# Kernel tuning notes

Measured on AMD Instinct MI355X. Metric: run time of the kernel, lower is better.

Reference implementation:

```python
import jax, jax.numpy as jnp
import numpy as np

EMBED = 1024
HEADS = 16
HEAD_DIM = EMBED // HEADS


def setup_inputs() -> dict:
    key = jax.random.key(0)
    ks = jax.random.split(key, 5)
    s = 0.02
    x = jax.random.normal(ks[0], (2, 2048, EMBED), dtype=jnp.float32)
    W_qkv = jax.random.normal(ks[1], (EMBED, 3 * EMBED), dtype=jnp.float32) * s
    b_qkv = jnp.zeros((3 * EMBED,), dtype=jnp.float32)
    W_proj = jax.random.normal(ks[2], (EMBED, EMBED), dtype=jnp.float32) * s
    b_proj = jnp.zeros((EMBED,), dtype=jnp.float32)
    return {"x": x, "W_qkv": W_qkv, "b_qkv": b_qkv, "W_proj": W_proj, "b_proj": b_proj}


def reference(x, W_qkv, b_qkv, W_proj, b_proj):
    B, N, _ = x.shape
    scale = HEAD_DIM ** -0.5
    qkv = x @ W_qkv + b_qkv                     # [B,N,3E]
    qkv = qkv.reshape(B, N, 3, HEADS, HEAD_DIM)
    q = qkv[:, :, 0].transpose(0, 2, 1, 3) * scale  # [B,H,N,D]
    k = qkv[:, :, 1].transpose(0, 2, 1, 3)
    v = qkv[:, :, 2].transpose(0, 2, 1, 3)
    attn = jnp.einsum('bhnd,bhmd->bhnm', q, k)  # [B,H,N,N]
    attn = jax.nn.softmax(attn, axis=-1)
    out = jnp.einsum('bhnm,bhmd->bhnd', attn, v)  # [B,H,N,D]
    out = out.transpose(0, 2, 1, 3).reshape(B, N, HEADS * HEAD_DIM)
    return out @ W_proj + b_proj
```

## Files before the change

### kernel.cpp

```cpp
#include <hip/hip_runtime.h>
#include <hip/hip_bf16.h>
#include <stdint.h>

typedef unsigned short u16;
typedef __bf16 bf16x8 __attribute__((ext_vector_type(8)));
typedef float f32x4 __attribute__((ext_vector_type(4)));
typedef float f32x16 __attribute__((ext_vector_type(16)));

__device__ __forceinline__ u16 f2bf(float f) {
    union { float f; unsigned u; } x; x.f = f;
    unsigned u = x.u;
    u += 0x7FFFu + ((u >> 16) & 1u);
    return (u16)(u >> 16);
}
__device__ __forceinline__ float bf2f(u16 h) {
    union { unsigned u; float f; } x; x.u = ((unsigned)h) << 16; return x.f;
}

typedef __attribute__((address_space(1))) void gvoid;
typedef __attribute__((address_space(3))) void lvoid;
__device__ __forceinline__ void gl2lds16(const void* g, void* l) {
    __builtin_amdgcn_global_load_lds((gvoid*)g, (lvoid*)l, 16, 0, 0);
}

__global__ __launch_bounds__(256) void prep_kernel(
    const float* __restrict__ x, u16* __restrict__ xb,
    const float* __restrict__ Wqkv, u16* __restrict__ wqkvT,
    const float* __restrict__ Wproj, u16* __restrict__ wprojT)
{
    __shared__ u16 tile[64][65];
    const int blk = blockIdx.x;
    const int tid = threadIdx.x;

    if (blk < 2048) {
        const size_t i = ((size_t)blk * 256 + tid) * 8;
        float4 a = *(const float4*)(x + i);
        float4 b = *(const float4*)(x + i + 4);
        ushort4 oa, ob;
        oa.x = f2bf(a.x); oa.y = f2bf(a.y); oa.z = f2bf(a.z); oa.w = f2bf(a.w);
        ob.x = f2bf(b.x); ob.y = f2bf(b.y); ob.z = f2bf(b.z); ob.w = f2bf(b.w);
        *(ushort4*)(xb + i) = oa;
        *(ushort4*)(xb + i + 4) = ob;
        return;
    }
    const float* in; u16* out; int rows, cols, bx, by;
    if (blk < 2816) { int t = blk - 2048; in = Wqkv;  out = wqkvT;  rows = 1024; cols = 3072; bx = t % 48; by = t / 48; }
    else            { int t = blk - 2816; in = Wproj; out = wprojT; rows = 1024; cols = 1024; bx = t % 16; by = t / 16; }
#pragma unroll
    for (int i = 0; i < 16; i++) {
        int e = i * 256 + tid;
        int r = e >> 6, c = e & 63;
        tile[r][c] = f2bf(in[(size_t)(by * 64 + r) * cols + bx * 64 + c]);
    }
    __syncthreads();
#pragma unroll
    for (int i = 0; i < 16; i++) {
        int e = i * 256 + tid;
        int r = e >> 6, c = e & 63;
        out[(size_t)(bx * 64 + r) * rows + by * 64 + c] = tile[c][r];
    }
}

__global__ __launch_bounds__(256) void gemm_qkv(
    const u16* __restrict__ A, const u16* __restrict__ Bt,
    const float* __restrict__ bias,
    u16* __restrict__ q, u16* __restrict__ ko, u16* __restrict__ vt)
{
    constexpr int K = 1024;
    __shared__ __align__(16) u16 smem[64 * 64 + 128 * 64];
    u16* sA = smem;
    u16* sB = smem + 4096;
    const int tid = threadIdx.x;
    const int wave = tid >> 6, lane = tid & 63;
    const int quad = lane >> 4, l16 = lane & 15;
    const int wm = (wave >> 1) * 32, wn = (wave & 1) * 64;
    const int m0 = blockIdx.y * 64, n0 = blockIdx.x * 128;
    const int srow = lane >> 3;
    const int scolz = ((lane & 7) ^ srow) * 8;

    f32x4 acc[2][4];
#pragma unroll
    for (int i = 0; i < 2; i++)
#pragma unroll
        for (int j = 0; j < 4; j++)
#pragma unroll
            for (int r = 0; r < 4; r++) acc[i][j][r] = 0.f;

    for (int kt = 0; kt < K; kt += 64) {
        __syncthreads();
#pragma unroll
        for (int t = 0; t < 2; t++) {
            int rb = wave * 16 + t * 8;
            gl2lds16(A + (size_t)(m0 + rb + srow) * K + kt + scolz, &sA[rb * 64]);
        }
#pragma unroll
        for (int t = 0; t < 4; t++) {
            int rb = wave * 32 + t * 8;
            gl2lds16(Bt + (size_t)(n0 + rb + srow) * K + kt + scolz, &sB[rb * 64]);
        }
        __syncthreads();
#pragma unroll
        for (int kk = 0; kk < 64; kk += 32) {
            bf16x8 af[2], bfr[4];
            int sl = (((kk >> 3) + quad) ^ (l16 & 7)) * 8;
#pragma unroll
            for (int t = 0; t < 2; t++)
                af[t] = *(const bf16x8*)&sA[(wm + t * 16 + l16) * 64 + sl];
#pragma unroll
            for (int t = 0; t < 4; t++)
                bfr[t] = *(const bf16x8*)&sB[(wn + t * 16 + l16) * 64 + sl];
#pragma unroll
            for (int i = 0; i < 2; i++)
#pragma unroll
                for (int j = 0; j < 4; j++)
                    acc[i][j] = __builtin_amdgcn_mfma_f32_16x16x32_bf16(
                        af[i], bfr[j], acc[i][j], 0, 0, 0);
        }
    }

    const float QSCALE = 0.18033688011112042f;
    const float sc = (n0 < 1024) ? QSCALE : 1.0f;
    __syncthreads();
#pragma unroll
    for (int i = 0; i < 2; i++) {
#pragma unroll
        for (int j = 0; j < 4; j++) {
            float bv = bias[n0 + wn + j * 16 + l16];
#pragma unroll
            for (int r = 0; r < 4; r++) {
                float v = (acc[i][j][r] + bv) * sc;
                smem[(wm + i * 16 + quad * 4 + r) * 132 + wn + j * 16 + l16] = f2bf(v);
            }
        }
    }
    __syncthreads();

    if (n0 < 2048) {
        u16* dst = (n0 < 1024) ? q : ko;
#pragma unroll
        for (int it = 0; it < 4; it++) {
            int c = it * 256 + tid;
            int m_l = c >> 4;
            int n8 = (c & 15) * 8;
            uint4 w = *(const uint4*)&smem[m_l * 132 + n8];
            int n = n0 + n8;
            int h = (n & 1023) >> 6, d = n & 63;
            int m = m0 + m_l;
            int b = m >> 11, t = m & 2047;
            *(uint4*)(dst + ((size_t)(b * 16 + h) * 2048 + t) * 64 + d) = w;
        }
    } else {
        constexpr int PERM[16] = {0,1,2,3, 8,9,10,11, 4,5,6,7, 12,13,14,15};
        int nv = n0 - 2048;
        int n_l = tid & 127, mh = tid >> 7;
        int hh = (nv >> 6) + (n_l >> 6);
        int d = n_l & 63;
        int bb = m0 >> 11, t0 = m0 & 2047;
        u16* vrow = vt + ((size_t)(bb * 16 + hh) * 64 + d) * 2048 + t0 + mh * 32;
#pragma unroll
        for (int it = 0; it < 4; it++) {
            int base = mh * 32 + it * 8;
            union { u16 s[8]; uint4 w; } pk;
#pragma unroll
            for (int i = 0; i < 8; i++) {
                int pos = base + i;
                int row = (pos & ~15) | PERM[pos & 15];
                pk.s[i] = smem[row * 132 + n_l];
            }
            *(uint4*)(vrow + it * 8) = pk.w;
        }
    }
}

__global__ __launch_bounds__(256, 4) void attn_kernel(
    const u16* __restrict__ q, const u16* __restrict__ ko,
    const u16* __restrict__ vt,
    u16* __restrict__ op0, u16* __restrict__ op1,
    float* __restrict__ lp0, float* __restrict__ lp1)
{
    __shared__ __align__(16) u16 sK[2][64 * 72];
    __shared__ __align__(16) u16 sV[2][64 * 72];

    const int tid = threadIdx.x;
    const int wave = tid >> 6, lane = tid & 63;
    const int l31 = lane & 31, hi = lane >> 5;

    const int lid = blockIdx.x;
    const int xcd = lid & 7, idx = lid >> 3;
    const int h = xcd * 2 + (idx & 1);
    const int b = (idx >> 1) & 1;
    const int q0 = ((idx >> 2) & 15) * 128;
    const int khalf = idx >> 6;
    const int kbase = khalf * 1024;
    const size_t bh = (size_t)(b * 16 + h);

    const u16* qp  = q  + bh * 2048 * 64;
    const u16* kp  = ko + bh * 2048 * 64;
    const u16* vtp = vt + bh * 64 * 2048;

    bf16x8 qf[4];
    {
        const u16* qrow = qp + (size_t)(q0 + wave * 32 + l31) * 64 + hi * 8;
#pragma unroll
        for (int d = 0; d < 4; d++)
            qf[d] = *(const bf16x8*)(qrow + d * 16);
    }

    const int sr0 = tid >> 3;
    const int sc0 = (tid & 7) * 8;
    const int sr1 = sr0 + 32;

    uint4 pk0 = *(const uint4*)(kp + (size_t)(kbase + sr0) * 64 + sc0);
    uint4 pk1 = *(const uint4*)(kp + (size_t)(kbase + sr1) * 64 + sc0);
    uint4 pv0 = *(const uint4*)(vtp + (size_t)sr0 * 2048 + kbase + sc0);
    uint4 pv1 = *(const uint4*)(vtp + (size_t)sr1 * 2048 + kbase + sc0);

    f32x16 accO[2];
#pragma unroll
    for (int d = 0; d < 2; d++)
#pragma unroll
        for (int r = 0; r < 16; r++) accO[d][r] = 0.f;
    float ls[4] = {0.f, 0.f, 0.f, 0.f};

    for (int t = 0; t < 16; ++t) {
        const int cur = t & 1;
        u16* sKc = &sK[cur][0];
        u16* sVc = &sV[cur][0];
        *(uint4*)&sKc[sr0 * 72 + sc0] = pk0;
        *(uint4*)&sKc[sr1 * 72 + sc0] = pk1;
        *(uint4*)&sVc[sr0 * 72 + sc0] = pv0;
        *(uint4*)&sVc[sr1 * 72 + sc0] = pv1;
        if (t < 15) {
            int nt = kbase + (t + 1) * 64;
            pk0 = *(const uint4*)(kp + (size_t)(nt + sr0) * 64 + sc0);
            pk1 = *(const uint4*)(kp + (size_t)(nt + sr1) * 64 + sc0);
            pv0 = *(const uint4*)(vtp + (size_t)sr0 * 2048 + nt + sc0);
            pv1 = *(const uint4*)(vtp + (size_t)sr1 * 2048 + nt + sc0);
        }
        __syncthreads();

#pragma unroll
        for (int rb = 0; rb < 2; rb++) {
            f32x16 S;
#pragma unroll
            for (int r = 0; r < 16; r++) S[r] = 0.f;
            const u16* krd = &sKc[(rb * 32 + l31) * 72 + hi * 8];
#pragma unroll
            for (int d = 0; d < 4; d++) {
                bf16x8 kf = *(const bf16x8*)(krd + d * 16);
                S = __builtin_amdgcn_mfma_f32_32x32x16_bf16(kf, qf[d], S, 0, 0, 0);
            }
            union { float f; unsigned u; } e[16];
#pragma unroll
            for (int r = 0; r < 16; r++) {
                e[r].f = __builtin_amdgcn_exp2f(S[r]);
                ls[r & 3] += e[r].f;
            }
#pragma unroll
            for (int ks2 = 0; ks2 < 2; ks2++) {
                union { unsigned u[4]; bf16x8 v; } pa;
#pragma unroll
                for (int s = 0; s < 4; s++) {
                    unsigned r0 = e[ks2 * 8 + 2 * s].u + 0x8000u;
                    unsigned r1 = e[ks2 * 8 + 2 * s + 1].u + 0x8000u;
                    pa.u[s] = (r1 & 0xFFFF0000u) | (r0 >> 16);
                }
                const int nb = rb * 32 + ks2 * 16 + hi * 8;
#pragma unroll
                for (int db = 0; db < 2; db++) {
                    bf16x8 vf = *(const bf16x8*)&sVc[(db * 32 + l31) * 72 + nb];
                    accO[db] = __builtin_amdgcn_mfma_f32_32x32x16_bf16(pa.v, vf, accO[db], 0, 0, 0);
                }
            }
        }
    }

    u16* op = khalf ? op1 : op0;
    float* lp = khalf ? lp1 : lp0;

    float lsum = (ls[0] + ls[1]) + (ls[2] + ls[3]);
    float ltot = lsum + __shfl_xor(lsum, 32, 64);
    int qq0 = q0 + wave * 32;
    if (hi == 0) lp[bh * 2048 + qq0 + l31] = ltot;

#pragma unroll
    for (int db = 0; db < 2; db++)
#pragma unroll
        for (int r = 0; r < 16; r++) {
            int tq = qq0 + (r & 3) + 8 * (r >> 2) + 4 * hi;
            size_t row = (size_t)b * 2048 + tq;
            op[row * 1024 + h * 64 + db * 32 + l31] = f2bf(accO[db][r]);
        }
}

__global__ __launch_bounds__(256) void combine_kernel(
    const u16* __restrict__ op0, const u16* __restrict__ op1,
    const float* __restrict__ lp0, const float* __restrict__ lp1,
    u16* __restrict__ ob)
{
    const size_t i = ((size_t)blockIdx.x * 256 + threadIdx.x) * 8;
    int m = (int)(i >> 10), e = (int)(i & 1023);
    int b = m >> 11, t = m & 2047, h = e >> 6;
    float inv = 1.f / (lp0[(size_t)(b * 16 + h) * 2048 + t] +
                       lp1[(size_t)(b * 16 + h) * 2048 + t]);
    union { uint4 w; u16 s[8]; } a, c, o;
    a.w = *(const uint4*)(op0 + i);
    c.w = *(const uint4*)(op1 + i);
#pragma unroll
    for (int k = 0; k < 8; k++)
        o.s[k] = f2bf((bf2f(a.s[k]) + bf2f(c.s[k])) * inv);
    *(uint4*)(ob + i) = o.w;
}

__global__ __launch_bounds__(256) void gemm_proj(
    const u16* __restrict__ A, const u16* __restrict__ Bt,
    const float* __restrict__ bias, float* __restrict__ out)
{
    constexpr int K = 1024;
    __shared__ __align__(16) u16 sA[32 * 64];
    __shared__ __align__(16) u16 sB[128 * 64];
    const int tid = threadIdx.x;
    const int wave = tid >> 6, lane = tid & 63;
    const int quad = lane >> 4, l16 = lane & 15;
    const int wn = wave * 32;

    const int lid = blockIdx.x;
    const int xcd = lid & 7, idx = lid >> 3;
    const int m0 = (xcd * 16 + (idx & 15)) * 32;
    const int n0 = (idx >> 4) * 128;

    const int srow = lane >> 3;
    const int scolz = ((lane & 7) ^ srow) * 8;

    f32x4 acc[2][2];
#pragma unroll
    for (int i = 0; i < 2; i++)
#pragma unroll
        for (int j = 0; j < 2; j++)
#pragma unroll
            for (int r = 0; r < 4; r++) acc[i][j][r] = 0.f;

    for (int kt = 0; kt < K; kt += 64) {
        __syncthreads();
        {
            int rb = wave * 8;
            gl2lds16(A + (size_t)(m0 + rb + srow) * K + kt + scolz, &sA[rb * 64]);
        }
#pragma unroll
        for (int t = 0; t < 4; t++) {
            int rb = wave * 32 + t * 8;
            gl2lds16(Bt + (size_t)(n0 + rb + srow) * K + kt + scolz, &sB[rb * 64]);
        }
        __syncthreads();
#pragma unroll
        for (int kk = 0; kk < 64; kk += 32) {
            bf16x8 af[2], bfr[2];
            int sl = (((kk >> 3) + quad) ^ (l16 & 7)) * 8;
#pragma unroll
            for (int t = 0; t < 2; t++)
                af[t] = *(const bf16x8*)&sA[(t * 16 + l16) * 64 + sl];
#pragma unroll
            for (int t = 0; t < 2; t++)
                bfr[t] = *(const bf16x8*)&sB[(wn + t * 16 + l16) * 64 + sl];
#pragma unroll
            for (int i = 0; i < 2; i++)
#pragma unroll
                for (int j = 0; j < 2; j++)
                    acc[i][j] = __builtin_amdgcn_mfma_f32_16x16x32_bf16(
                        af[i], bfr[j], acc[i][j], 0, 0, 0);
        }
    }

#pragma unroll
    for (int i = 0; i < 2; i++) {
#pragma unroll
        for (int j = 0; j < 2; j++) {
            int n = n0 + wn + j * 16 + l16;
            float bv = bias[n];
#pragma unroll
            for (int r = 0; r < 4; r++) {
                int m = m0 + i * 16 + quad * 4 + r;
                out[(size_t)m * 1024 + n] = acc[i][j][r] + bv;
            }
        }
    }
}

extern "C" void kernel_launch(void* const* d_in, const int* in_sizes, int n_in,
                              void* d_out, int out_size, void* d_ws, size_t ws_size,
                              hipStream_t stream) {
    const float* x     = (const float*)d_in[0];
    const float* Wqkv  = (const float*)d_in[1];
    const float* bqkv  = (const float*)d_in[2];
    const float* Wproj = (const float*)d_in[3];
    const float* bproj = (const float*)d_in[4];
    float* out = (float*)d_out;
    char* ws = (char*)d_ws;

    u16* wqkvT  = (u16*)(ws);
    u16* wprojT = (u16*)(ws +  6291456);
    u16* xb     = (u16*)(ws +  8388608);
    u16* qb     = (u16*)(ws + 16777216);
    u16* kb     = (u16*)(ws + 25165824);
    u16* vtb    = (u16*)(ws + 33554432);
    u16* ob     = (u16*)(ws + 41943040);

    u16*   op0 = ob;
    u16*   op1 = xb;
    float* lp0 = (float*)wqkvT;
    float* lp1 = (float*)(ws + 262144);

    prep_kernel<<<dim3(3072), 256, 0, stream>>>(x, xb, Wqkv, wqkvT, Wproj, wprojT);
    gemm_qkv<<<dim3(24, 64), 256, 0, stream>>>(xb, wqkvT, bqkv, qb, kb, vtb);
    attn_kernel<<<dim3(1024), 256, 0, stream>>>(qb, kb, vtb, op0, op1, lp0, lp1);
    combine_kernel<<<dim3(2048), 256, 0, stream>>>(op0, op1, lp0, lp1, ob);
    gemm_proj<<<dim3(1024), 256, 0, stream>>>(ob, wprojT, bproj, out);
}
```

Before: 185.7 us.

## Fuse split-K combine into attention kernel via per-tile arrival counter

Drops the separate combine kernel. Each attention block bumps an atomic counter for its query tile after writing its partial output and row sum. The second block to arrive reads the other half's partial output and row sums, then writes the normalized bf16 result straight into the projection input. This removes one kernel launch and one full pass over both partial buffers. In exchange it adds a counter memset, thread fences, and scattered 2-byte global loads and stores in the attention epilogue.

After: 285.4 us. 1.54x slower.

```diff
diff --git a/kernel.cpp b/kernel.cpp
--- a/kernel.cpp
+++ b/kernel.cpp
@@ -176,10 +176,12 @@
     const u16* __restrict__ q, const u16* __restrict__ ko,
     const u16* __restrict__ vt,
     u16* __restrict__ op0, u16* __restrict__ op1,
-    float* __restrict__ lp0, float* __restrict__ lp1)
+    float* __restrict__ lp0, float* __restrict__ lp1,
+    int* __restrict__ cnt, u16* __restrict__ obf)
 {
     __shared__ __align__(16) u16 sK[2][64 * 72];
     __shared__ __align__(16) u16 sV[2][64 * 72];
+    __shared__ int sOld;
 
     const int tid = threadIdx.x;
     const int wave = tid >> 6, lane = tid & 63;
@@ -189,10 +191,12 @@
     const int xcd = lid & 7, idx = lid >> 3;
     const int h = xcd * 2 + (idx & 1);
     const int b = (idx >> 1) & 1;
-    const int q0 = ((idx >> 2) & 15) * 128;
+    const int qt = (idx >> 2) & 15;
+    const int q0 = qt * 128;
     const int khalf = idx >> 6;
     const int kbase = khalf * 1024;
     const size_t bh = (size_t)(b * 16 + h);
+    const int tileid = (int)bh * 16 + qt;
 
     const u16* qp  = q  + bh * 2048 * 64;
     const u16* kp  = ko + bh * 2048 * 64;
@@ -291,25 +295,32 @@
             size_t row = (size_t)b * 2048 + tq;
             op[row * 1024 + h * 64 + db * 32 + l31] = f2bf(accO[db][r]);
         }
-}
-
-__global__ __launch_bounds__(256) void combine_kernel(
-    const u16* __restrict__ op0, const u16* __restrict__ op1,
-    const float* __restrict__ lp0, const float* __restrict__ lp1,
-    u16* __restrict__ ob)
-{
-    const size_t i = ((size_t)blockIdx.x * 256 + threadIdx.x) * 8;
-    int m = (int)(i >> 10), e = (int)(i & 1023);
-    int b = m >> 11, t = m & 2047, h = e >> 6;
-    float inv = 1.f / (lp0[(size_t)(b * 16 + h) * 2048 + t] +
-                       lp1[(size_t)(b * 16 + h) * 2048 + t]);
-    union { uint4 w; u16 s[8]; } a, c, o;
-    a.w = *(const uint4*)(op0 + i);
-    c.w = *(const uint4*)(op1 + i);
-#pragma unroll
-    for (int k = 0; k < 8; k++)
-        o.s[k] = f2bf((bf2f(a.s[k]) + bf2f(c.s[k])) * inv);
-    *(uint4*)(ob + i) = o.w;
+
+    __syncthreads();
+    if (tid == 0) {
+        __threadfence();
+        sOld = atomicAdd(&cnt[tileid], 1);
+    }
+    __syncthreads();
+    if (sOld == 0) return;
+
+    __threadfence();
+    const u16*   oo = khalf ? op0 : op1;
+    const float* lo = khalf ? lp0 : lp1;
+    float lot = lo[bh * 2048 + qq0 + l31];
+
+#pragma unroll
+    for (int db = 0; db < 2; db++)
+#pragma unroll
+        for (int r = 0; r < 16; r++) {
+            int rloc = (r & 3) + 8 * (r >> 2) + 4 * hi;
+            float denom = __shfl(ltot, rloc, 32) + __shfl(lot, rloc, 32);
+            float inv = 1.f / denom;
+            size_t row = (size_t)b * 2048 + qq0 + rloc;
+            size_t a = row * 1024 + h * 64 + db * 32 + l31;
+            float v = (bf2f(f2bf(accO[db][r])) + bf2f(oo[a])) * inv;
+            obf[a] = f2bf(v);
+        }
 }
 
 __global__ __launch_bounds__(256) void gemm_proj(
@@ -409,10 +420,11 @@
     u16*   op1 = xb;
     float* lp0 = (float*)wqkvT;
     float* lp1 = (float*)(ws + 262144);
+    int*   cnt = (int*)(ws + 1048576);
 
     prep_kernel<<<dim3(3072), 256, 0, stream>>>(x, xb, Wqkv, wqkvT, Wproj, wprojT);
     gemm_qkv<<<dim3(24, 64), 256, 0, stream>>>(xb, wqkvT, bqkv, qb, kb, vtb);
-    attn_kernel<<<dim3(1024), 256, 0, stream>>>(qb, kb, vtb, op0, op1, lp0, lp1);
-    combine_kernel<<<dim3(2048), 256, 0, stream>>>(op0, op1, lp0, lp1, ob);
+    hipMemsetAsync(cnt, 0, 512 * sizeof(int), stream);
+    attn_kernel<<<dim3(1024), 256, 0, stream>>>(qb, kb, vtb, op0, op1, lp0, lp1, cnt, ob);
     gemm_proj<<<dim3(1024), 256, 0, stream>>>(ob, wprojT, bproj, out);
 }
```
